# Performance work log

Measured on AMD Instinct MI355X. Metric: run time of the kernel, lower is better.

## Reference

```python
import jax, jax.numpy as jnp
import numpy as np

EMBED = 384   # embeddingSize
BLOCK = 256   # blockSize (max T, also actual T here)
HEAD = 64     # headSize
B = 512
NEG_INF = -1e9  # stands in for float('-inf'); safe under fp16/bf16 via finite large value


def setup_inputs() -> dict:
    key = jax.random.key(0)
    k1, k2, k3, k4 = jax.random.split(key, 4)
    input = jax.random.normal(k1, (B, BLOCK, EMBED), dtype=jnp.float32)
    # nn.Linear(EMBED, HEAD, bias=False) weights, stored transposed for x @ W
    s = 1.0 / np.sqrt(EMBED)
    Wk = jax.random.uniform(k2, (EMBED, HEAD), dtype=jnp.float32, minval=-s, maxval=s)
    Wq = jax.random.uniform(k3, (EMBED, HEAD), dtype=jnp.float32, minval=-s, maxval=s)
    Wv = jax.random.uniform(k4, (EMBED, HEAD), dtype=jnp.float32, minval=-s, maxval=s)
    return {"input": input, "Wk": Wk, "Wq": Wq, "Wv": Wv}


def reference(input, Wk, Wq, Wv):
    B_, T, C = input.shape
    k = input @ Wk  # (B, T, H)
    q = input @ Wq  # (B, T, H)
    v = input @ Wv  # (B, T, H)
    # NOTE: original scales by C**-0.5 where C = embedding size (384), not head size.
    scale = jnp.asarray(C, input.dtype) ** -0.5
    weight = jnp.einsum('bth,bsh->bts', q, k) * scale  # (B, Tq, Tk)
    causal = jnp.tril(jnp.ones((T, T), dtype=bool))    # tril[:T,:T]
    weight = jnp.where(causal, weight, NEG_INF)
    # NOTE: original applies softmax over dim=1 (the QUERY axis), faithfully reproduced.
    weight = jax.nn.softmax(weight, axis=1)
    # dropout is identity in eval mode (deterministic reference)
    output = jnp.einsum('bts,bsh->bth', weight, v)     # (B, T, H)
    return output
```

## Files before the change

### kernel.cpp

```cpp
#include <hip/hip_runtime.h>
#include <hip/hip_bf16.h>

#define TT 256
#define CE 384
#define HD 64

typedef __attribute__((ext_vector_type(8))) short short8v;
typedef __attribute__((ext_vector_type(4))) float float4v;
typedef __attribute__((ext_vector_type(4))) unsigned int uint4v;
typedef __attribute__((ext_vector_type(4))) unsigned short ushort4v;

#define SCALE 0.05103103630798287f

__device__ __forceinline__ unsigned short f2bf(float f) {
    unsigned int u = __float_as_uint(f);
    unsigned int r = (u + 0x7FFFu + ((u >> 16) & 1u)) >> 16;
    return (unsigned short)r;
}
__device__ __forceinline__ unsigned int pk2(float a, float b) {
    return (unsigned int)f2bf(a) | ((unsigned int)f2bf(b) << 16);
}

__device__ __forceinline__ int adr8(int row, int col) {
    return row * 128 + ((((col >> 3) ^ (row & 7)) & 7) << 4) + ((col & 7) << 1);
}
__device__ __forceinline__ int adr16(int row, int col) {
    return row * 256 + ((((col >> 3) ^ (row & 15)) & 15) << 4) + ((col & 7) << 1);
}

__global__ void wprep(const float* __restrict__ Wk, const float* __restrict__ Wq,
                      const float* __restrict__ Wv, unsigned short* __restrict__ Wt) {
    int idx = blockIdx.x * 256 + threadIdx.x;
    if (idx >= 3 * HD * CE) return;
    int w = idx / (HD * CE);
    int rem = idx - w * (HD * CE);
    int h = rem / CE;
    int c = rem - h * CE;
    const float* W = (w == 0) ? Wk : (w == 1) ? Wq : Wv;
    Wt[idx] = f2bf(W[c * HD + h]);
}

__global__ __launch_bounds__(512, 2)
void fused(const float* __restrict__ X, const unsigned short* __restrict__ Wt,
           float* __restrict__ out) {
    extern __shared__ char lds[];
    char* Qs   = lds;
    char* Ks   = lds + 32768;
    char* Vts0 = lds + 65536;
    char* Wts  = lds + 98304;
    char* Xs   = Wts;
    char* Ws   = Wts + 32768;

    const int b = blockIdx.x;
    const int tid = threadIdx.x;
    const int w = tid >> 6, l = tid & 63;
    const int l15 = l & 15, lq = l >> 4;

    const int tg = w & 3, nh = w >> 2;

    const float4v fzero = {0.f, 0.f, 0.f, 0.f};
    float4v acc[4][6];
    #pragma unroll
    for (int i = 0; i < 4; ++i)
        #pragma unroll
        for (int j = 0; j < 6; ++j) acc[i][j] = fzero;

    const float* Xb = X + (long)b * TT * CE;

    int xt[4], xk[4], wn[3], wk[3];
    #pragma unroll
    for (int j = 0; j < 4; ++j) { int ci = j * 512 + tid; xt[j] = ci >> 3; xk[j] = ci & 7; }
    #pragma unroll
    for (int j = 0; j < 3; ++j) { int ci = j * 512 + tid; wn[j] = ci >> 3; wk[j] = ci & 7; }

    float4 xr[4][2];
    uint4v wreg[3];

    auto load_chunk = [&](int kk) {
        #pragma unroll
        for (int j = 0; j < 4; ++j) {
            const float* src = Xb + xt[j] * CE + kk + xk[j] * 8;
            xr[j][0] = *(const float4*)src;
            xr[j][1] = *(const float4*)(src + 4);
        }
        #pragma unroll
        for (int j = 0; j < 3; ++j)
            wreg[j] = *(const uint4v*)(Wt + wn[j] * CE + kk + wk[j] * 8);
    };
    auto store_chunk = [&]() {
        #pragma unroll
        for (int j = 0; j < 4; ++j) {
            uint4v p = {pk2(xr[j][0].x, xr[j][0].y), pk2(xr[j][0].z, xr[j][0].w),
                        pk2(xr[j][1].x, xr[j][1].y), pk2(xr[j][1].z, xr[j][1].w)};
            *(uint4v*)(Xs + xt[j] * 128 + (((xk[j] ^ (xt[j] & 7)) & 7) << 4)) = p;
        }
        #pragma unroll
        for (int j = 0; j < 3; ++j)
            *(uint4v*)(Ws + wn[j] * 128 + (((wk[j] ^ (wn[j] & 7)) & 7) << 4)) = wreg[j];
    };

    load_chunk(0);
    for (int kc = 0; kc < 6; ++kc) {
        __syncthreads();
        store_chunk();
        if (kc < 5) load_chunk((kc + 1) * 64);
        __syncthreads();
        #pragma unroll
        for (int ks = 0; ks < 2; ++ks) {
            short8v a[4];
            #pragma unroll
            for (int rt = 0; rt < 4; ++rt)
                a[rt] = *(const short8v*)(Xs + adr8(tg * 64 + rt * 16 + l15, ks * 32 + lq * 8));
            #pragma unroll
            for (int nt = 0; nt < 6; ++nt) {
                short8v bb = *(const short8v*)(Ws + adr8(nh * 96 + nt * 16 + l15, ks * 32 + lq * 8));
                #pragma unroll
                for (int rt = 0; rt < 4; ++rt)
                    acc[rt][nt] = __builtin_amdgcn_mfma_f32_16x16x32_bf16(a[rt], bb, acc[rt][nt], 0, 0, 0);
            }
        }
    }

    __syncthreads();

    #pragma unroll
    for (int rt = 0; rt < 4; ++rt) {
        const int t0 = tg * 64 + rt * 16 + lq * 4;
        #pragma unroll
        for (int nt = 0; nt < 6; ++nt) {
            const int n = nh * 96 + nt * 16 + l15;
            if (n < 64) {
                #pragma unroll
                for (int r = 0; r < 4; ++r)
                    *(unsigned short*)(Ks + adr8(t0 + r, n)) = f2bf(acc[rt][nt][r]);
            } else if (n < 128) {
                const int h = n - 64;
                #pragma unroll
                for (int r = 0; r < 4; ++r)
                    *(unsigned short*)(Qs + adr8(t0 + r, h)) = f2bf(acc[rt][nt][r]);
            } else {
                const int h = n - 128;
                char* vbase = Vts0 + (t0 >> 7) * 16384;
                const int sl = t0 & 127;
                ushort4v pv;
                pv[0] = f2bf(acc[rt][nt][0]);
                pv[1] = f2bf(acc[rt][nt][1]);
                pv[2] = f2bf(acc[rt][nt][2]);
                pv[3] = f2bf(acc[rt][nt][3]);
                *(ushort4v*)(vbase + adr16(h, sl)) = pv;
            }
        }
    }

    float4v o[2][4];
    #pragma unroll
    for (int i = 0; i < 2; ++i)
        #pragma unroll
        for (int j = 0; j < 4; ++j) o[i][j] = fzero;

    for (int sb = 0; sb < 2; ++sb) {
        const int s0 = sb * 128;
        __syncthreads();

        float4v z[16];
        #pragma unroll
        for (int tt = 0; tt < 16; ++tt) z[tt] = fzero;
        #pragma unroll
        for (int ks = 0; ks < 2; ++ks) {
            short8v ak = *(const short8v*)(Ks + adr8(s0 + w * 16 + l15, ks * 32 + lq * 8));
            #pragma unroll
            for (int tt = 0; tt < 16; ++tt) {
                short8v bq = *(const short8v*)(Qs + adr8(tt * 16 + l15, ks * 32 + lq * 8));
                z[tt] = __builtin_amdgcn_mfma_f32_16x16x32_bf16(ak, bq, z[tt], 0, 0, 0);
            }
        }

        float inv[4];
        const int sgb = s0 + w * 16 + lq * 4;
        #pragma unroll
        for (int r = 0; r < 4; ++r) {
            const int s = sgb + r;
            float mm = -1e30f;
            #pragma unroll
            for (int tt = 0; tt < 16; ++tt) {
                int t = tt * 16 + l15;
                float v = (t >= s) ? z[tt][r] * SCALE : -1e30f;
                z[tt][r] = v;
                mm = fmaxf(mm, v);
            }
            mm = fmaxf(mm, __shfl_xor(mm, 1));
            mm = fmaxf(mm, __shfl_xor(mm, 2));
            mm = fmaxf(mm, __shfl_xor(mm, 4));
            mm = fmaxf(mm, __shfl_xor(mm, 8));
            float ss = 0.f;
            #pragma unroll
            for (int tt = 0; tt < 16; ++tt) {
                float p = (z[tt][r] > -1e29f) ? __expf(z[tt][r] - mm) : 0.f;
                z[tt][r] = p;
                ss += p;
            }
            ss += __shfl_xor(ss, 1);
            ss += __shfl_xor(ss, 2);
            ss += __shfl_xor(ss, 4);
            ss += __shfl_xor(ss, 8);
            inv[r] = 1.f / ss;
        }

        #pragma unroll
        for (int tt = 0; tt < 16; ++tt) {
            int t = tt * 16 + l15;
            int col = w * 16 + lq * 4;
            ushort4v pw;
            pw[0] = f2bf(z[tt][0] * inv[0]);
            pw[1] = f2bf(z[tt][1] * inv[1]);
            pw[2] = f2bf(z[tt][2] * inv[2]);
            pw[3] = f2bf(z[tt][3] * inv[3]);
            *(ushort4v*)(Wts + adr16(t, col)) = pw;
        }
        __syncthreads();

        const char* vb = Vts0 + sb * 16384;
        #pragma unroll
        for (int ks = 0; ks < 4; ++ks) {
            short8v aw0 = *(const short8v*)(Wts + adr16(w * 32 + l15,      ks * 32 + lq * 8));
            short8v aw1 = *(const short8v*)(Wts + adr16(w * 32 + 16 + l15, ks * 32 + lq * 8));
            #pragma unroll
            for (int ht = 0; ht < 4; ++ht) {
                short8v bv = *(const short8v*)(vb + adr16(ht * 16 + l15, ks * 32 + lq * 8));
                o[0][ht] = __builtin_amdgcn_mfma_f32_16x16x32_bf16(aw0, bv, o[0][ht], 0, 0, 0);
                o[1][ht] = __builtin_amdgcn_mfma_f32_16x16x32_bf16(aw1, bv, o[1][ht], 0, 0, 0);
            }
        }
    }

    #pragma unroll
    for (int rt = 0; rt < 2; ++rt)
        #pragma unroll
        for (int ht = 0; ht < 4; ++ht) {
            int t0 = w * 32 + rt * 16 + lq * 4;
            int h = ht * 16 + l15;
            #pragma unroll
            for (int r = 0; r < 4; ++r)
                out[((long)b * TT + t0 + r) * HD + h] = o[rt][ht][r];
        }
}

extern "C" void kernel_launch(void* const* d_in, const int* in_sizes, int n_in,
                              void* d_out, int out_size, void* d_ws, size_t ws_size,
                              hipStream_t stream) {
    const float* X  = (const float*)d_in[0];
    const float* Wk = (const float*)d_in[1];
    const float* Wq = (const float*)d_in[2];
    const float* Wv = (const float*)d_in[3];
    float* out = (float*)d_out;

    unsigned short* Wt = (unsigned short*)d_ws;

    (void)hipFuncSetAttribute(reinterpret_cast<const void*>(fused),
                              hipFuncAttributeMaxDynamicSharedMemorySize, 163840);

    wprep<<<288, 256, 0, stream>>>(Wk, Wq, Wv, Wt);
    fused<<<512, 512, 163840, stream>>>(X, Wt, out);
}
```

Measured before the change: 73.86 us.

## Double-buffer global loads in projection GEMM with explicit lgkm barriers

The projection GEMM's global-to-register prefetch now keeps two register buffers (A/B), so global loads are issued two chunks ahead of their LDS store. The loop is fully unrolled, and its __syncthreads calls are replaced by s_waitcnt lgkmcnt(0), a raw s_barrier and a scheduling barrier. This is meant to hide global memory latency behind the MFMA phases. The bf16 conversion also switches to the __float2bfloat16 intrinsic. The extra buffers raise register pressure and could lower occupancy.

```diff
diff --git a/kernel.cpp b/kernel.cpp
--- a/kernel.cpp
+++ b/kernel.cpp
@@ -13,9 +13,9 @@
 #define SCALE 0.05103103630798287f
 
 __device__ __forceinline__ unsigned short f2bf(float f) {
-    unsigned int u = __float_as_uint(f);
-    unsigned int r = (u + 0x7FFFu + ((u >> 16) & 1u)) >> 16;
-    return (unsigned short)r;
+    union { __hip_bfloat16 b; unsigned short u; } cv;
+    cv.b = __float2bfloat16(f);
+    return cv.u;
 }
 __device__ __forceinline__ unsigned int pk2(float a, float b) {
     return (unsigned int)f2bf(a) | ((unsigned int)f2bf(b) << 16);
@@ -73,38 +73,54 @@
     #pragma unroll
     for (int j = 0; j < 3; ++j) { int ci = j * 512 + tid; wn[j] = ci >> 3; wk[j] = ci & 7; }
 
-    float4 xr[4][2];
-    uint4v wreg[3];
-
-    auto load_chunk = [&](int kk) {
+    float4 xrA[4][2]; uint4v wrA[3];
+    float4 xrB[4][2]; uint4v wrB[3];
+
+    auto issueA = [&](int kk) {
         #pragma unroll
         for (int j = 0; j < 4; ++j) {
             const float* src = Xb + xt[j] * CE + kk + xk[j] * 8;
-            xr[j][0] = *(const float4*)src;
-            xr[j][1] = *(const float4*)(src + 4);
+            xrA[j][0] = *(const float4*)src;
+            xrA[j][1] = *(const float4*)(src + 4);
         }
         #pragma unroll
         for (int j = 0; j < 3; ++j)
-            wreg[j] = *(const uint4v*)(Wt + wn[j] * CE + kk + wk[j] * 8);
-    };
-    auto store_chunk = [&]() {
+            wrA[j] = *(const uint4v*)(Wt + wn[j] * CE + kk + wk[j] * 8);
+    };
+    auto issueB = [&](int kk) {
         #pragma unroll
         for (int j = 0; j < 4; ++j) {
-            uint4v p = {pk2(xr[j][0].x, xr[j][0].y), pk2(xr[j][0].z, xr[j][0].w),
-                        pk2(xr[j][1].x, xr[j][1].y), pk2(xr[j][1].z, xr[j][1].w)};
+            const float* src = Xb + xt[j] * CE + kk + xk[j] * 8;
+            xrB[j][0] = *(const float4*)src;
+            xrB[j][1] = *(const float4*)(src + 4);
+        }
+        #pragma unroll
+        for (int j = 0; j < 3; ++j)
+            wrB[j] = *(const uint4v*)(Wt + wn[j] * CE + kk + wk[j] * 8);
+    };
+    auto storeA = [&]() {
+        #pragma unroll
+        for (int j = 0; j < 4; ++j) {
+            uint4v p = {pk2(xrA[j][0].x, xrA[j][0].y), pk2(xrA[j][0].z, xrA[j][0].w),
+                        pk2(xrA[j][1].x, xrA[j][1].y), pk2(xrA[j][1].z, xrA[j][1].w)};
             *(uint4v*)(Xs + xt[j] * 128 + (((xk[j] ^ (xt[j] & 7)) & 7) << 4)) = p;
         }
         #pragma unroll
         for (int j = 0; j < 3; ++j)
-            *(uint4v*)(Ws + wn[j] * 128 + (((wk[j] ^ (wn[j] & 7)) & 7) << 4)) = wreg[j];
-    };
-
-    load_chunk(0);
-    for (int kc = 0; kc < 6; ++kc) {
-        __syncthreads();
-        store_chunk();
-        if (kc < 5) load_chunk((kc + 1) * 64);
-        __syncthreads();
+            *(uint4v*)(Ws + wn[j] * 128 + (((wk[j] ^ (wn[j] & 7)) & 7) << 4)) = wrA[j];
+    };
+    auto storeB = [&]() {
+        #pragma unroll
+        for (int j = 0; j < 4; ++j) {
+            uint4v p = {pk2(xrB[j][0].x, xrB[j][0].y), pk2(xrB[j][0].z, xrB[j][0].w),
+                        pk2(xrB[j][1].x, xrB[j][1].y), pk2(xrB[j][1].z, xrB[j][1].w)};
+            *(uint4v*)(Xs + xt[j] * 128 + (((xk[j] ^ (xt[j] & 7)) & 7) << 4)) = p;
+        }
+        #pragma unroll
+        for (int j = 0; j < 3; ++j)
+            *(uint4v*)(Ws + wn[j] * 128 + (((wk[j] ^ (wn[j] & 7)) & 7) << 4)) = wrB[j];
+    };
+    auto mfma_phase = [&]() {
         #pragma unroll
         for (int ks = 0; ks < 2; ++ks) {
             short8v a[4];
@@ -119,9 +135,30 @@
                     acc[rt][nt] = __builtin_amdgcn_mfma_f32_16x16x32_bf16(a[rt], bb, acc[rt][nt], 0, 0, 0);
             }
         }
+    };
+
+    #define LGKM0_BAR() do {                                          \
+        asm volatile("s_waitcnt lgkmcnt(0)" ::: "memory");            \
+        __builtin_amdgcn_s_barrier();                                 \
+        __builtin_amdgcn_sched_barrier(0);                            \
+    } while (0)
+
+    issueA(0);
+    issueB(64);
+    #pragma unroll
+    for (int kc2 = 0; kc2 < 3; ++kc2) {
+        storeA();
+        if (kc2 < 2) issueA((2 * kc2 + 2) * 64);
+        LGKM0_BAR();
+        mfma_phase();
+        LGKM0_BAR();
+        storeB();
+        if (kc2 < 2) issueB((2 * kc2 + 3) * 64);
+        LGKM0_BAR();
+        mfma_phase();
+        LGKM0_BAR();
     }
-
-    __syncthreads();
+    #undef LGKM0_BAR
 
     #pragma unroll
     for (int rt = 0; rt < 4; ++rt) {
```

Result: slower. 77.68 us (+5.2%).

## Use 1024-thread blocks processing two batches each with double-buffered global prefetch

Applied to the files above, without the earlier changes.

Moves the fused kernel to 1024-thread workgroups, launched as 256 blocks that each process two batch elements in turn. Global loads of X and W are double-buffered in registers, and the next batch's first chunks are prefetched during the attention phase. Each wave now owns 16 keys, so the attention step handles all 256 keys in one pass with a wider swizzled LDS layout. Barriers become explicit lgkmcnt waits plus s_barrier. The trade-offs are fewer resident workgroups, more register pressure at 1024 threads, and a slower library bf16 conversion in place of the hand-written one.

```diff
diff --git a/kernel.cpp b/kernel.cpp
--- a/kernel.cpp
+++ b/kernel.cpp
@@ -13,9 +13,9 @@
 #define SCALE 0.05103103630798287f
 
 __device__ __forceinline__ unsigned short f2bf(float f) {
-    unsigned int u = __float_as_uint(f);
-    unsigned int r = (u + 0x7FFFu + ((u >> 16) & 1u)) >> 16;
-    return (unsigned short)r;
+    union { __hip_bfloat16 b; unsigned short u; } cv;
+    cv.b = __float2bfloat16(f);
+    return cv.u;
 }
 __device__ __forceinline__ unsigned int pk2(float a, float b) {
     return (unsigned int)f2bf(a) | ((unsigned int)f2bf(b) << 16);
@@ -24,9 +24,15 @@
 __device__ __forceinline__ int adr8(int row, int col) {
     return row * 128 + ((((col >> 3) ^ (row & 7)) & 7) << 4) + ((col & 7) << 1);
 }
-__device__ __forceinline__ int adr16(int row, int col) {
-    return row * 256 + ((((col >> 3) ^ (row & 15)) & 15) << 4) + ((col & 7) << 1);
-}
+__device__ __forceinline__ int adr32(int row, int col) {
+    return row * 512 + ((((col >> 3) ^ (row & 31)) & 31) << 4) + ((col & 7) << 1);
+}
+
+#define BAR() do {                                            \
+    asm volatile("s_waitcnt lgkmcnt(0)" ::: "memory");        \
+    __builtin_amdgcn_s_barrier();                             \
+    __builtin_amdgcn_sched_barrier(0);                        \
+} while (0)
 
 __global__ void wprep(const float* __restrict__ Wk, const float* __restrict__ Wq,
                       const float* __restrict__ Wv, unsigned short* __restrict__ Wt) {
@@ -40,146 +46,159 @@
     Wt[idx] = f2bf(W[c * HD + h]);
 }
 
-__global__ __launch_bounds__(512, 2)
+__global__ __launch_bounds__(1024, 4)
 void fused(const float* __restrict__ X, const unsigned short* __restrict__ Wt,
            float* __restrict__ out) {
     extern __shared__ char lds[];
-    char* Qs   = lds;
-    char* Ks   = lds + 32768;
-    char* Vts0 = lds + 65536;
-    char* Wts  = lds + 98304;
-    char* Xs   = Wts;
-    char* Ws   = Wts + 32768;
-
-    const int b = blockIdx.x;
+    char* Vts = lds;
+    char* Qs  = lds + 32768;
+    char* Ks  = lds + 65536;
+    char* Xs  = lds + 98304;
+    char* Ws  = lds + 131072;
+    char* Wts = lds + 32768;
+
     const int tid = threadIdx.x;
     const int w = tid >> 6, l = tid & 63;
     const int l15 = l & 15, lq = l >> 4;
-
-    const int tg = w & 3, nh = w >> 2;
+    const int tg = w & 7, nh = w >> 3;
+
+    const int xt0 = tid >> 3,        xk0 = tid & 7;
+    const int xt1 = 128 + (tid >> 3), xk1 = tid & 7;
+    const int wn0 = tid >> 3,        wk0 = tid & 7;
+    const int wn1 = 128 + (tid >> 3), wk1 = tid & 7;
+    const bool wp = (tid < 512);
+
+    float4 xrA[2][2]; uint4v wrA[2];
+    float4 xrB[2][2]; uint4v wrB[2];
+
+    auto issueA = [&](const float* xb, int kk) {
+        const float* s0 = xb + xt0 * CE + kk + xk0 * 8;
+        xrA[0][0] = *(const float4*)s0;  xrA[0][1] = *(const float4*)(s0 + 4);
+        const float* s1 = xb + xt1 * CE + kk + xk1 * 8;
+        xrA[1][0] = *(const float4*)s1;  xrA[1][1] = *(const float4*)(s1 + 4);
+        wrA[0] = *(const uint4v*)(Wt + wn0 * CE + kk + wk0 * 8);
+        if (wp) wrA[1] = *(const uint4v*)(Wt + wn1 * CE + kk + wk1 * 8);
+    };
+    auto issueB = [&](const float* xb, int kk) {
+        const float* s0 = xb + xt0 * CE + kk + xk0 * 8;
+        xrB[0][0] = *(const float4*)s0;  xrB[0][1] = *(const float4*)(s0 + 4);
+        const float* s1 = xb + xt1 * CE + kk + xk1 * 8;
+        xrB[1][0] = *(const float4*)s1;  xrB[1][1] = *(const float4*)(s1 + 4);
+        wrB[0] = *(const uint4v*)(Wt + wn0 * CE + kk + wk0 * 8);
+        if (wp) wrB[1] = *(const uint4v*)(Wt + wn1 * CE + kk + wk1 * 8);
+    };
+    auto storeA = [&]() {
+        uint4v p0 = {pk2(xrA[0][0].x, xrA[0][0].y), pk2(xrA[0][0].z, xrA[0][0].w),
+                     pk2(xrA[0][1].x, xrA[0][1].y), pk2(xrA[0][1].z, xrA[0][1].w)};
+        *(uint4v*)(Xs + xt0 * 128 + (((xk0 ^ (xt0 & 7)) & 7) << 4)) = p0;
+        uint4v p1 = {pk2(xrA[1][0].x, xrA[1][0].y), pk2(xrA[1][0].z, xrA[1][0].w),
+                     pk2(xrA[1][1].x, xrA[1][1].y), pk2(xrA[1][1].z, xrA[1][1].w)};
+        *(uint4v*)(Xs + xt1 * 128 + (((xk1 ^ (xt1 & 7)) & 7) << 4)) = p1;
+        *(uint4v*)(Ws + wn0 * 128 + (((wk0 ^ (wn0 & 7)) & 7) << 4)) = wrA[0];
+        if (wp) *(uint4v*)(Ws + wn1 * 128 + (((wk1 ^ (wn1 & 7)) & 7) << 4)) = wrA[1];
+    };
+    auto storeB = [&]() {
+        uint4v p0 = {pk2(xrB[0][0].x, xrB[0][0].y), pk2(xrB[0][0].z, xrB[0][0].w),
+                     pk2(xrB[0][1].x, xrB[0][1].y), pk2(xrB[0][1].z, xrB[0][1].w)};
+        *(uint4v*)(Xs + xt0 * 128 + (((xk0 ^ (xt0 & 7)) & 7) << 4)) = p0;
+        uint4v p1 = {pk2(xrB[1][0].x, xrB[1][0].y), pk2(xrB[1][0].z, xrB[1][0].w),
+                     pk2(xrB[1][1].x, xrB[1][1].y), pk2(xrB[1][1].z, xrB[1][1].w)};
+        *(uint4v*)(Xs + xt1 * 128 + (((xk1 ^ (xt1 & 7)) & 7) << 4)) = p1;
+        *(uint4v*)(Ws + wn0 * 128 + (((wk0 ^ (wn0 & 7)) & 7) << 4)) = wrB[0];
+        if (wp) *(uint4v*)(Ws + wn1 * 128 + (((wk1 ^ (wn1 & 7)) & 7) << 4)) = wrB[1];
+    };
 
     const float4v fzero = {0.f, 0.f, 0.f, 0.f};
-    float4v acc[4][6];
-    #pragma unroll
-    for (int i = 0; i < 4; ++i)
-        #pragma unroll
-        for (int j = 0; j < 6; ++j) acc[i][j] = fzero;
-
-    const float* Xb = X + (long)b * TT * CE;
-
-    int xt[4], xk[4], wn[3], wk[3];
-    #pragma unroll
-    for (int j = 0; j < 4; ++j) { int ci = j * 512 + tid; xt[j] = ci >> 3; xk[j] = ci & 7; }
-    #pragma unroll
-    for (int j = 0; j < 3; ++j) { int ci = j * 512 + tid; wn[j] = ci >> 3; wk[j] = ci & 7; }
-
-    float4 xr[4][2];
-    uint4v wreg[3];
-
-    auto load_chunk = [&](int kk) {
-        #pragma unroll
-        for (int j = 0; j < 4; ++j) {
-            const float* src = Xb + xt[j] * CE + kk + xk[j] * 8;
-            xr[j][0] = *(const float4*)src;
-            xr[j][1] = *(const float4*)(src + 4);
-        }
-        #pragma unroll
-        for (int j = 0; j < 3; ++j)
-            wreg[j] = *(const uint4v*)(Wt + wn[j] * CE + kk + wk[j] * 8);
-    };
-    auto store_chunk = [&]() {
-        #pragma unroll
-        for (int j = 0; j < 4; ++j) {
-            uint4v p = {pk2(xr[j][0].x, xr[j][0].y), pk2(xr[j][0].z, xr[j][0].w),
-                        pk2(xr[j][1].x, xr[j][1].y), pk2(xr[j][1].z, xr[j][1].w)};
-            *(uint4v*)(Xs + xt[j] * 128 + (((xk[j] ^ (xt[j] & 7)) & 7) << 4)) = p;
-        }
-        #pragma unroll
-        for (int j = 0; j < 3; ++j)
-            *(uint4v*)(Ws + wn[j] * 128 + (((wk[j] ^ (wn[j] & 7)) & 7) << 4)) = wreg[j];
-    };
-
-    load_chunk(0);
-    for (int kc = 0; kc < 6; ++kc) {
-        __syncthreads();
-        store_chunk();
-        if (kc < 5) load_chunk((kc + 1) * 64);
-        __syncthreads();
+    float4v acc[2][6];
+
+    auto mfma_phase = [&]() {
         #pragma unroll
         for (int ks = 0; ks < 2; ++ks) {
-            short8v a[4];
-            #pragma unroll
-            for (int rt = 0; rt < 4; ++rt)
-                a[rt] = *(const short8v*)(Xs + adr8(tg * 64 + rt * 16 + l15, ks * 32 + lq * 8));
+            short8v a0 = *(const short8v*)(Xs + adr8(tg * 32 + l15,      ks * 32 + lq * 8));
+            short8v a1 = *(const short8v*)(Xs + adr8(tg * 32 + 16 + l15, ks * 32 + lq * 8));
             #pragma unroll
             for (int nt = 0; nt < 6; ++nt) {
                 short8v bb = *(const short8v*)(Ws + adr8(nh * 96 + nt * 16 + l15, ks * 32 + lq * 8));
-                #pragma unroll
-                for (int rt = 0; rt < 4; ++rt)
-                    acc[rt][nt] = __builtin_amdgcn_mfma_f32_16x16x32_bf16(a[rt], bb, acc[rt][nt], 0, 0, 0);
-            }
-        }
-    }
-
-    __syncthreads();
+                acc[0][nt] = __builtin_amdgcn_mfma_f32_16x16x32_bf16(a0, bb, acc[0][nt], 0, 0, 0);
+                acc[1][nt] = __builtin_amdgcn_mfma_f32_16x16x32_bf16(a1, bb, acc[1][nt], 0, 0, 0);
+            }
+        }
+    };
+
+    const int b0 = blockIdx.x;
+    issueA(X + (long)b0 * TT * CE, 0);
+    issueB(X + (long)b0 * TT * CE, 64);
 
     #pragma unroll
-    for (int rt = 0; rt < 4; ++rt) {
-        const int t0 = tg * 64 + rt * 16 + lq * 4;
-        #pragma unroll
-        for (int nt = 0; nt < 6; ++nt) {
-            const int n = nh * 96 + nt * 16 + l15;
-            if (n < 64) {
-                #pragma unroll
-                for (int r = 0; r < 4; ++r)
-                    *(unsigned short*)(Ks + adr8(t0 + r, n)) = f2bf(acc[rt][nt][r]);
-            } else if (n < 128) {
-                const int h = n - 64;
-                #pragma unroll
-                for (int r = 0; r < 4; ++r)
-                    *(unsigned short*)(Qs + adr8(t0 + r, h)) = f2bf(acc[rt][nt][r]);
-            } else {
-                const int h = n - 128;
-                char* vbase = Vts0 + (t0 >> 7) * 16384;
-                const int sl = t0 & 127;
-                ushort4v pv;
-                pv[0] = f2bf(acc[rt][nt][0]);
-                pv[1] = f2bf(acc[rt][nt][1]);
-                pv[2] = f2bf(acc[rt][nt][2]);
-                pv[3] = f2bf(acc[rt][nt][3]);
-                *(ushort4v*)(vbase + adr16(h, sl)) = pv;
-            }
-        }
-    }
-
-    float4v o[2][4];
-    #pragma unroll
-    for (int i = 0; i < 2; ++i)
-        #pragma unroll
-        for (int j = 0; j < 4; ++j) o[i][j] = fzero;
-
-    for (int sb = 0; sb < 2; ++sb) {
-        const int s0 = sb * 128;
-        __syncthreads();
+    for (int bb = 0; bb < 2; ++bb) {
+        const int bat = b0 + bb * 256;
+        const float* Xb = X + (long)bat * TT * CE;
+
+        #pragma unroll
+        for (int i = 0; i < 2; ++i)
+            #pragma unroll
+            for (int j = 0; j < 6; ++j) acc[i][j] = fzero;
+
+        #pragma unroll
+        for (int kc2 = 0; kc2 < 3; ++kc2) {
+            storeA();
+            if (kc2 < 2) issueA(Xb, (2 * kc2 + 2) * 64);
+            BAR();
+            mfma_phase();
+            BAR();
+            storeB();
+            if (kc2 < 2) issueB(Xb, (2 * kc2 + 3) * 64);
+            BAR();
+            mfma_phase();
+            BAR();
+        }
+
+        #pragma unroll
+        for (int rt = 0; rt < 2; ++rt) {
+            const int t0 = tg * 32 + rt * 16 + lq * 4;
+            #pragma unroll
+            for (int nt = 0; nt < 6; ++nt) {
+                const int n = nh * 96 + nt * 16 + l15;
+                if (n < 64) {
+                    #pragma unroll
+                    for (int r = 0; r < 4; ++r)
+                        *(unsigned short*)(Ks + adr8(t0 + r, n)) = f2bf(acc[rt][nt][r]);
+                } else if (n < 128) {
+                    const int h = n - 64;
+                    #pragma unroll
+                    for (int r = 0; r < 4; ++r)
+                        *(unsigned short*)(Qs + adr8(t0 + r, h)) = f2bf(acc[rt][nt][r]);
+                } else {
+                    const int h = n - 128;
+                    ushort4v pv;
+                    pv[0] = f2bf(acc[rt][nt][0]);
+                    pv[1] = f2bf(acc[rt][nt][1]);
+                    pv[2] = f2bf(acc[rt][nt][2]);
+                    pv[3] = f2bf(acc[rt][nt][3]);
+                    *(ushort4v*)(Vts + adr32(h, t0)) = pv;
+                }
+            }
+        }
+        BAR();
 
         float4v z[16];
         #pragma unroll
         for (int tt = 0; tt < 16; ++tt) z[tt] = fzero;
         #pragma unroll
         for (int ks = 0; ks < 2; ++ks) {
-            short8v ak = *(const short8v*)(Ks + adr8(s0 + w * 16 + l15, ks * 32 + lq * 8));
+            short8v ak = *(const short8v*)(Ks + adr8(w * 16 + l15, ks * 32 + lq * 8));
             #pragma unroll
             for (int tt = 0; tt < 16; ++tt) {
                 short8v bq = *(const short8v*)(Qs + adr8(tt * 16 + l15, ks * 32 + lq * 8));
                 z[tt] = __builtin_amdgcn_mfma_f32_16x16x32_bf16(ak, bq, z[tt], 0, 0, 0);
             }
         }
+        BAR();
 
         float inv[4];
-        const int sgb = s0 + w * 16 + lq * 4;
         #pragma unroll
         for (int r = 0; r < 4; ++r) {
-            const int s = sgb + r;
+            const int s = w * 16 + lq * 4 + r;
             float mm = -1e30f;
             #pragma unroll
             for (int tt = 0; tt < 16; ++tt) {
@@ -208,41 +227,45 @@
 
         #pragma unroll
         for (int tt = 0; tt < 16; ++tt) {
-            int t = tt * 16 + l15;
-            int col = w * 16 + lq * 4;
+            const int t = tt * 16 + l15;
+            const int col = w * 16 + lq * 4;
             ushort4v pw;
             pw[0] = f2bf(z[tt][0] * inv[0]);
             pw[1] = f2bf(z[tt][1] * inv[1]);
             pw[2] = f2bf(z[tt][2] * inv[2]);
             pw[3] = f2bf(z[tt][3] * inv[3]);
-            *(ushort4v*)(Wts + adr16(t, col)) = pw;
-        }
-        __syncthreads();
-
-        const char* vb = Vts0 + sb * 16384;
-        #pragma unroll
-        for (int ks = 0; ks < 4; ++ks) {
-            short8v aw0 = *(const short8v*)(Wts + adr16(w * 32 + l15,      ks * 32 + lq * 8));
-            short8v aw1 = *(const short8v*)(Wts + adr16(w * 32 + 16 + l15, ks * 32 + lq * 8));
+            *(ushort4v*)(Wts + adr32(t, col)) = pw;
+        }
+
+        if (bb == 0) {
+            const float* Xb1 = X + (long)(b0 + 256) * TT * CE;
+            issueA(Xb1, 0);
+            issueB(Xb1, 64);
+        }
+        BAR();
+
+        float4v o[4];
+        #pragma unroll
+        for (int ht = 0; ht < 4; ++ht) o[ht] = fzero;
+        #pragma unroll
+        for (int ks = 0; ks < 8; ++ks) {
+            short8v aw = *(const short8v*)(Wts + adr32(w * 16 + l15, ks * 32 + lq * 8));
             #pragma unroll
             for (int ht = 0; ht < 4; ++ht) {
-                short8v bv = *(const short8v*)(vb + adr16(ht * 16 + l15, ks * 32 + lq * 8));
-                o[0][ht] = __builtin_amdgcn_mfma_f32_16x16x32_bf16(aw0, bv, o[0][ht], 0, 0, 0);
-                o[1][ht] = __builtin_amdgcn_mfma_f32_16x16x32_bf16(aw1, bv, o[1][ht], 0, 0, 0);
-            }
-        }
+                short8v bv = *(const short8v*)(Vts + adr32(ht * 16 + l15, ks * 32 + lq * 8));
+                o[ht] = __builtin_amdgcn_mfma_f32_16x16x32_bf16(aw, bv, o[ht], 0, 0, 0);
+            }
+        }
+
+        float* ob = out + (long)bat * TT * HD;
+        #pragma unroll
+        for (int ht = 0; ht < 4; ++ht)
+            #pragma unroll
+            for (int r = 0; r < 4; ++r)
+                ob[(w * 16 + lq * 4 + r) * HD + ht * 16 + l15] = o[ht][r];
+
+        if (bb == 0) BAR();
     }
-
-    #pragma unroll
-    for (int rt = 0; rt < 2; ++rt)
-        #pragma unroll
-        for (int ht = 0; ht < 4; ++ht) {
-            int t0 = w * 32 + rt * 16 + lq * 4;
-            int h = ht * 16 + l15;
-            #pragma unroll
-            for (int r = 0; r < 4; ++r)
-                out[((long)b * TT + t0 + r) * HD + h] = o[rt][ht][r];
-        }
 }
 
 extern "C" void kernel_launch(void* const* d_in, const int* in_sizes, int n_in,
@@ -260,5 +283,5 @@
                               hipFuncAttributeMaxDynamicSharedMemorySize, 163840);
 
     wprep<<<288, 256, 0, stream>>>(Wk, Wq, Wv, Wt);
-    fused<<<512, 512, 163840, stream>>>(X, Wt, out);
-}
+    fused<<<256, 1024, 163840, stream>>>(X, Wt, out);
+}
```

Measured after the change: 172.1 us. +133.0%, slower.
